# Performance work log

Hardware: AMD Instinct MI355X
Metric: run time of the kernel (lower is better)

The kernel has to match this reference:

```python
import jax, jax.numpy as jnp
import numpy as np

N_NODES = 100000
N_EDGES = 3200000
F_IN, F_HID, F_OUT = 32, 32, 16


def spline_conv(x, edge_index, edge_attr, W, root, bias):
    """SplineConv, dim=1, kernel_size=2, degree=1, open spline, aggr='mean'.
    Basis weights over the 2 kernel slots are (1-u, u) for pseudo u in [0,1).
    W: [2, Fin, Fout], root: [Fin, Fout], bias: [Fout]."""
    src, dst = edge_index[0], edge_index[1]
    u = jnp.clip(edge_attr[:, 0:1], 0.0, 1.0)          # [E,1]
    x_src = x[src]                                      # [E,Fin] gather
    msg = (1.0 - u) * (x_src @ W[0]) + u * (x_src @ W[1])  # [E,Fout]
    agg = jax.ops.segment_sum(msg, dst, num_segments=x.shape[0])
    cnt = jax.ops.segment_sum(jnp.ones((msg.shape[0],), dtype=x.dtype), dst,
                              num_segments=x.shape[0])
    agg = agg / jnp.maximum(cnt, 1.0)[:, None]          # mean aggregation
    return agg + x @ root + bias


def setup_inputs() -> dict:
    key = jax.random.key(0)
    ks = jax.random.split(key, 9)
    x = jax.random.normal(ks[0], (N_NODES, F_IN), dtype=jnp.float32)
    edge_index = jax.random.randint(ks[1], (2, N_EDGES), 0, N_NODES, dtype=jnp.int64)
    edge_attr = jax.random.uniform(ks[2], (N_EDGES, 1), dtype=jnp.float32)
    s1 = 1.0 / np.sqrt(F_IN)
    s2 = 1.0 / np.sqrt(F_HID)
    W1 = jax.random.normal(ks[3], (2, F_IN, F_HID), dtype=jnp.float32) * s1
    root1 = jax.random.normal(ks[4], (F_IN, F_HID), dtype=jnp.float32) * s1
    b1 = jnp.zeros((F_HID,), dtype=jnp.float32)
    W2 = jax.random.normal(ks[5], (2, F_HID, F_OUT), dtype=jnp.float32) * s2
    root2 = jax.random.normal(ks[6], (F_HID, F_OUT), dtype=jnp.float32) * s2
    b2 = jnp.zeros((F_OUT,), dtype=jnp.float32)
    return {"x": x, "edge_index": edge_index, "edge_attr": edge_attr,
            "W1": W1, "root1": root1, "b1": b1,
            "W2": W2, "root2": root2, "b2": b2}


def reference(x, edge_index, edge_attr, W1, root1, b1, W2, root2, b2):
    # dropout is identity in eval mode
    h = jax.nn.relu(spline_conv(x, edge_index, edge_attr, W1, root1, b1))
    h = spline_conv(h, edge_index, edge_attr, W2, root2, b2)
    return jax.nn.log_softmax(h, axis=1)
```

## Files before the change

### kernel.cpp

```cpp
#include <hip/hip_runtime.h>
#include <math.h>

#define NN 100000
#define NE 3200000
#define BSH 6
#define BSZ 64
#define NBKT 1563
#define CAP 2560
#define STILE 8192
#define NTBS 391
#define NPB 1563
#define TST 68
#define NOFF (NBKT + 1)
#define OS2W 392

#define FMA4(a, s, v) { (a).x += (s)*(v).x; (a).y += (s)*(v).y; (a).z += (s)*(v).z; (a).w += (s)*(v).w; }

typedef float v2f __attribute__((ext_vector_type(2)));

__device__ __forceinline__ unsigned fp8pack4(float a, float b, float c, float d) {
    int r = __builtin_amdgcn_cvt_pk_fp8_f32(a, b, 0, false);
    r = __builtin_amdgcn_cvt_pk_fp8_f32(c, d, r, true);
    return (unsigned)r;
}

#define LDE(pp, vv, idx) { int e_ = (idx); \
    if (e_ < cn) { pp = (unsigned)pks[cs + e_]; vv = x1[(size_t)(pp >> 15) * 8 + j]; } \
    else { pp = 0u; vv = 0u; } }
#define ACC(pp, vv) { float u_ = (float)((pp) & 511u) * (1.f / 511.f); \
    v2f lo_ = __builtin_amdgcn_cvt_pk_f32_fp8((vv), false); \
    v2f hi_ = __builtin_amdgcn_cvt_pk_f32_fp8((vv), true); \
    T0 += lo_.x; B0 += u_ * lo_.x;  T1 += lo_.y; B1 += u_ * lo_.y; \
    T2 += hi_.x; B2 += u_ * hi_.x;  T3 += hi_.y; B3 += u_ * hi_.y; }

#define WALK_BODY() \
    int r = t >> 3, j = t & 7; \
    int cs = coff[r], cn = ccnt[r]; \
    float T0=0,T1=0,T2=0,T3=0,B0=0,B1=0,B2=0,B3=0; \
    unsigned pa0, pa1, pa2, pa3, pb0, pb1, pb2, pb3; \
    unsigned va0, va1, va2, va3, vb0, vb1, vb2, vb3; \
    LDE(pa0, va0, 0) LDE(pa1, va1, 1) LDE(pa2, va2, 2) LDE(pa3, va3, 3) \
    LDE(pb0, vb0, 4) LDE(pb1, vb1, 5) LDE(pb2, vb2, 6) LDE(pb3, vb3, 7) \
    for (int k = 0; k < cn; k += 8) { \
        ACC(pa0, va0) ACC(pa1, va1) ACC(pa2, va2) ACC(pa3, va3) \
        LDE(pa0, va0, k + 8)  LDE(pa1, va1, k + 9)  LDE(pa2, va2, k + 10) LDE(pa3, va3, k + 11) \
        ACC(pb0, vb0) ACC(pb1, vb1) ACC(pb2, vb2) ACC(pb3, vb3) \
        LDE(pb0, vb0, k + 12) LDE(pb1, vb1, k + 13) LDE(pb2, vb2, k + 14) LDE(pb3, vb3, k + 15) \
    } \
    __syncthreads();                       \
    ((float4*)(tb + r * TST + 4 * j))[0]      = make_float4(T0, T1, T2, T3); \
    ((float4*)(tb + r * TST + 32 + 4 * j))[0] = make_float4(B0, B1, B2, B3); \
    __syncthreads();

__global__ __launch_bounds__(512, 6) void sp_k(
    const int* __restrict__ ei, const float* __restrict__ ea,
    const float* __restrict__ x, const float* __restrict__ R, const float* __restrict__ b,
    int* __restrict__ pk, unsigned short* __restrict__ offs,
    unsigned* __restrict__ xb, float* __restrict__ xr)
{
    __shared__ __align__(16) union {
        struct { int h[2048]; int staged[STILE]; } sc;
        struct { float Rs[1024]; float xs[64 * 33]; } pp;
    } sm;
    int t = threadIdx.x;

    if (blockIdx.x < NTBS) {
        int* h = sm.sc.h;
        for (int i = t; i < 2048; i += 512) h[i] = 0;
        __syncthreads();
        int e0 = blockIdx.x * STILE;
        int cntblk = NE - e0; if (cntblk > STILE) cntblk = STILE;
        unsigned pck[16]; int bk[16], rk[16];
        #pragma unroll
        for (int i = 0; i < 16; i++) {
            int e = e0 + i * 512 + t;
            bk[i] = -1;
            if (e < NE) {
                int s = ei[e];
                int d = ei[NE + e];
                float u = fminf(fmaxf(ea[e], 0.f), 1.f);
                unsigned uq = __float2uint_rn(u * 511.f);
                bk[i] = d >> BSH;
                pck[i] = ((unsigned)s << 15) | ((unsigned)(d & (BSZ - 1)) << 9) | uq;
                rk[i] = atomicAdd(&h[bk[i]], 1);
            }
        }
        __syncthreads();
        int4 hc = ((const int4*)h)[t];
        int s4 = hc.x + hc.y + hc.z + hc.w;
        int lane = t & 63, wv = t >> 6;
        int inc = s4;
        #pragma unroll
        for (int ofs = 1; ofs < 64; ofs <<= 1) {
            int v = __shfl_up(inc, ofs);
            if (lane >= ofs) inc += v;
        }
        int* wsum = sm.sc.staged;
        if (lane == 63) wsum[wv] = inc;
        __syncthreads();
        int base = 0;
        #pragma unroll
        for (int i = 0; i < 8; i++) { int v = wsum[i]; if (i < wv) base += v; }
        int ex = base + inc - s4;
        __syncthreads();
        ((int4*)h)[t] = make_int4(ex, ex + hc.x, ex + hc.x + hc.y, ex + hc.x + hc.y + hc.z);
        __syncthreads();
        for (int k = t; k < NOFF; k += 512)
            offs[(size_t)blockIdx.x * NOFF + k] = (unsigned short)h[k];
        __syncthreads();
        #pragma unroll
        for (int i = 0; i < 16; i++)
            if (bk[i] >= 0) sm.sc.staged[h[bk[i]] + rk[i]] = (int)pck[i];
        __syncthreads();
        int* seg = pk + (size_t)blockIdx.x * STILE;
        for (int i = t; i * 4 < cntblk; i += 512)
            ((int4*)seg)[i] = ((const int4*)sm.sc.staged)[i];
    } else {
        for (int i = t; i < 1024; i += 512) sm.pp.Rs[i] = R[i];
        int nb = (blockIdx.x - NTBS) * 64;
        for (int i = t; i < 2048; i += 512) {
            int n = nb + (i >> 5);
            sm.pp.xs[(i >> 5) * 33 + (i & 31)] = (n < NN) ? x[n * 32 + (i & 31)] : 0.f;
        }
        __syncthreads();
        int local = t >> 3, c = t & 7;
        int n = nb + local;
        float4 a2 = make_float4(0.f, 0.f, 0.f, 0.f);
        #pragma unroll
        for (int k = 0; k < 32; k++) {
            float xk = sm.pp.xs[local * 33 + k];
            float4 r = ((const float4*)sm.pp.Rs)[k * 8 + c];
            FMA4(a2, xk, r);
        }
        if (n < NN) {
            float4 bb = ((const float4*)b)[c];
            a2.x += bb.x; a2.y += bb.y; a2.z += bb.z; a2.w += bb.w;
            ((float4*)xr)[n * 8 + c] = a2;
            xb[n * 8 + c] = fp8pack4(sm.pp.xs[local * 33 + c * 4 + 0],
                                     sm.pp.xs[local * 33 + c * 4 + 1],
                                     sm.pp.xs[local * 33 + c * 4 + 2],
                                     sm.pp.xs[local * 33 + c * 4 + 3]);
        }
    }
}

__global__ __launch_bounds__(256) void tr_k(
    const unsigned short* __restrict__ offs, unsigned* __restrict__ offs2)
{
    __shared__ unsigned short st[64][68];
    int kt = blockIdx.x % 25;
    int tt = blockIdx.x / 25;
    int t = threadIdx.x;
    for (int i = t; i < 64 * 66; i += 256) {
        int r = i / 66, c = i % 66;
        int row = tt * 64 + r, k = kt * 64 + c;
        st[r][c] = (row < NTBS && k < NOFF) ? offs[(size_t)row * NOFF + k] : (unsigned short)0;
    }
    __syncthreads();
    for (int i = t; i < 64 * 64; i += 256) {
        int kl = i >> 6, tl = i & 63;
        int k = kt * 64 + kl, row = tt * 64 + tl;
        if (k < NBKT && row < NTBS) {
            unsigned o0 = st[tl][kl];
            unsigned cnt = (unsigned)st[tl][kl + 1] - o0;
            offs2[(size_t)k * OS2W + row] = o0 | (cnt << 16);
        }
    }
}

__global__ __launch_bounds__(512, 8) void srt_k(
    const int* __restrict__ pk, const unsigned* __restrict__ offs2,
    int* __restrict__ pk2, int* __restrict__ cnt2)
{
    __shared__ int ccnt[BSZ], coff[BSZ], wsum[8];
    __shared__ __align__(16) int staged[CAP];
    __shared__ __align__(16) int pks[CAP];
    int t = threadIdx.x;
    int bkt = blockIdx.x;
    if (t < BSZ) ccnt[t] = 0;

    int cnt = 0, o0 = 0;
    if (t < NTBS) {
        unsigned pc = offs2[(size_t)bkt * OS2W + t];
        o0 = (int)(pc & 0xFFFFu);
        cnt = (int)(pc >> 16);
    }
    int lane = t & 63, wv = t >> 6;
    int inc = cnt;
    #pragma unroll
    for (int ofs = 1; ofs < 64; ofs <<= 1) {
        int v = __shfl_up(inc, ofs);
        if (lane >= ofs) inc += v;
    }
    if (lane == 63) wsum[wv] = inc;
    __syncthreads();
    int base = 0, tot = 0;
    #pragma unroll
    for (int i = 0; i < 8; i++) { int v = wsum[i]; tot += v; if (i < wv) base += v; }
    int dst = base + inc - cnt;
    int ne = tot < CAP ? tot : CAP;
    if (dst + cnt > CAP) { cnt = CAP - dst; if (cnt < 0) cnt = 0; }
    const int* seg = pk + (size_t)t * STILE + o0;
    int i2 = 0;
    for (; i2 + 4 <= cnt; i2 += 4) {
        int v0 = seg[i2], v1 = seg[i2 + 1], v2 = seg[i2 + 2], v3 = seg[i2 + 3];
        staged[dst + i2] = v0; staged[dst + i2 + 1] = v1;
        staged[dst + i2 + 2] = v2; staged[dst + i2 + 3] = v3;
    }
    for (; i2 < cnt; i2++) staged[dst + i2] = seg[i2];
    __syncthreads();

    unsigned er[5]; int rk[5];
    #pragma unroll
    for (int i = 0; i < 5; i++) {
        int e = i * 512 + t;
        rk[i] = -1;
        if (e < ne) {
            er[i] = (unsigned)staged[e];
            rk[i] = atomicAdd(&ccnt[(er[i] >> 9) & (BSZ - 1)], 1);
        }
    }
    __syncthreads();
    if (t < BSZ) {
        int v = ccnt[t], sc = v;
        #pragma unroll
        for (int ofs = 1; ofs < 64; ofs <<= 1) {
            int nn = __shfl_up(sc, ofs);
            if (t >= ofs) sc += nn;
        }
        coff[t] = sc - v;
    }
    __syncthreads();
    #pragma unroll
    for (int i = 0; i < 5; i++)
        if (rk[i] >= 0) pks[coff[(er[i] >> 9) & (BSZ - 1)] + rk[i]] = (int)er[i];
    if (t < BSZ) cnt2[bkt * BSZ + t] = ccnt[t];
    __syncthreads();

    int n4 = (ne + 3) >> 2;
    int4* dp = (int4*)(pk2 + (size_t)bkt * CAP);
    for (int i = t; i < n4; i += 512) dp[i] = ((const int4*)pks)[i];
}

__global__ __launch_bounds__(512, 8) void agg1_k(
    const int* __restrict__ pk2, const int* __restrict__ cnt2,
    const unsigned* __restrict__ xb, const float* __restrict__ W,
    const float* __restrict__ R2, const float* __restrict__ b2,
    const float* __restrict__ xr, unsigned* __restrict__ hb, float* __restrict__ hr)
{
    __shared__ float Wc[2048];
    __shared__ float R2s[512];
    __shared__ int ccnt[BSZ], coff[BSZ];
    __shared__ int smne;
    __shared__ __align__(16) char smraw[BSZ * TST * 4];
    __shared__ float hs[BSZ * 33];
    int* pks = (int*)smraw;
    float* tb = (float*)smraw;

    int t = threadIdx.x;
    for (int i = t; i < 1024; i += 512) {
        float w0 = W[i];
        Wc[i] = w0;
        Wc[1024 + i] = W[1024 + i] - w0;
    }
    if (t < 512) R2s[t] = R2[t];

    int bkt = blockIdx.x;
    if (t < BSZ) {
        int v = cnt2[bkt * BSZ + t];
        ccnt[t] = v;
        int sc = v;
        #pragma unroll
        for (int ofs = 1; ofs < 64; ofs <<= 1) {
            int nn = __shfl_up(sc, ofs);
            if (t >= ofs) sc += nn;
        }
        coff[t] = sc - v;
        if (t == 63) smne = sc;
    }
    __syncthreads();
    int ne = smne; if (ne > CAP) ne = CAP;
    {
        int n4 = (ne + 3) >> 2;
        const int4* sp4 = (const int4*)(pk2 + (size_t)bkt * CAP);
        for (int i = t; i < n4; i += 512) ((int4*)pks)[i] = sp4[i];
    }
    __syncthreads();

    const unsigned* x1 = xb;
    WALK_BODY()

    {
        int row = t >> 3, cc = t & 7;
        int n = bkt * BSZ + row;
        float inv = 1.f / fmaxf((float)ccnt[row], 1.f);
        float4 acc = make_float4(0.f, 0.f, 0.f, 0.f);
        #pragma unroll
        for (int k = 0; k < 32; k++) {
            float sa = tb[row * TST + k];
            float4 w = ((const float4*)Wc)[k * 8 + cc];
            FMA4(acc, sa, w);
        }
        #pragma unroll
        for (int k = 0; k < 32; k++) {
            float sb = tb[row * TST + 32 + k];
            float4 w = ((const float4*)Wc)[(32 + k) * 8 + cc];
            FMA4(acc, sb, w);
        }
        float h0 = 0.f, h1 = 0.f, h2 = 0.f, h3 = 0.f;
        if (n < NN) {
            float4 rr = ((const float4*)xr)[n * 8 + cc];
            h0 = fmaxf(acc.x * inv + rr.x, 0.f);
            h1 = fmaxf(acc.y * inv + rr.y, 0.f);
            h2 = fmaxf(acc.z * inv + rr.z, 0.f);
            h3 = fmaxf(acc.w * inv + rr.w, 0.f);
            hb[n * 8 + cc] = fp8pack4(h0, h1, h2, h3);
        }
        hs[row * 33 + cc * 4 + 0] = h0;
        hs[row * 33 + cc * 4 + 1] = h1;
        hs[row * 33 + cc * 4 + 2] = h2;
        hs[row * 33 + cc * 4 + 3] = h3;
    }
    __syncthreads();

    #pragma unroll
    for (int p = 0; p < 2; p++) {
        int idx = p * 512 + t;
        int row = idx >> 4, f = idx & 15;
        int n = bkt * BSZ + row;
        if (n < NN) {
            float o = 0.f;
            #pragma unroll
            for (int k = 0; k < 32; k++) o += hs[row * 33 + k] * R2s[k * 16 + f];
            hr[n * 16 + f] = o + b2[f];
        }
    }
}

__global__ __launch_bounds__(512, 8) void agg2_k(
    const int* __restrict__ pk2, const int* __restrict__ cnt2,
    const unsigned* __restrict__ hb, const float* __restrict__ W,
    const float* __restrict__ hr, float* __restrict__ out)
{
    __shared__ float Wc[1024];
    __shared__ int ccnt[BSZ], coff[BSZ];
    __shared__ int smne;
    __shared__ __align__(16) char smraw[BSZ * TST * 4];
    int* pks = (int*)smraw;
    float* tb = (float*)smraw;

    int t = threadIdx.x;
    if (t < 512) {
        float w0 = W[t];
        Wc[t] = w0;
        Wc[512 + t] = W[512 + t] - w0;
    }
    int bkt = blockIdx.x;
    if (t < BSZ) {
        int v = cnt2[bkt * BSZ + t];
        ccnt[t] = v;
        int sc = v;
        #pragma unroll
        for (int ofs = 1; ofs < 64; ofs <<= 1) {
            int nn = __shfl_up(sc, ofs);
            if (t >= ofs) sc += nn;
        }
        coff[t] = sc - v;
        if (t == 63) smne = sc;
    }
    __syncthreads();
    int ne = smne; if (ne > CAP) ne = CAP;
    {
        int n4 = (ne + 3) >> 2;
        const int4* sp4 = (const int4*)(pk2 + (size_t)bkt * CAP);
        for (int i = t; i < n4; i += 512) ((int4*)pks)[i] = sp4[i];
    }
    __syncthreads();

    const unsigned* x1 = hb;
    WALK_BODY()

    #pragma unroll
    for (int p = 0; p < 2; p++) {
        int row = p * 32 + (t >> 4), f = t & 15;
        int n = bkt * BSZ + row;
        float inv = 1.f / fmaxf((float)ccnt[row], 1.f);
        float o = 0.f;
        #pragma unroll
        for (int k = 0; k < 32; k++) o += tb[row * TST + k] * Wc[k * 16 + f];
        #pragma unroll
        for (int k = 0; k < 32; k++) o += tb[row * TST + 32 + k] * Wc[(32 + k) * 16 + f];
        if (n < NN) {
            o = o * inv + hr[n * 16 + f];
            float m = o;
            #pragma unroll
            for (int ofs = 8; ofs; ofs >>= 1) m = fmaxf(m, __shfl_xor(m, ofs, 16));
            float sm = expf(o - m);
            #pragma unroll
            for (int ofs = 8; ofs; ofs >>= 1) sm += __shfl_xor(sm, ofs, 16);
            out[n * 16 + f] = o - (m + logf(sm));
        }
    }
}

extern "C" void kernel_launch(void* const* d_in, const int* in_sizes, int n_in,
                              void* d_out, int out_size, void* d_ws, size_t ws_size,
                              hipStream_t stream) {
    const float* x     = (const float*)d_in[0];
    const int*   ei    = (const int*)d_in[1];
    const float* ea    = (const float*)d_in[2];
    const float* W1    = (const float*)d_in[3];
    const float* root1 = (const float*)d_in[4];
    const float* b1    = (const float*)d_in[5];
    const float* W2    = (const float*)d_in[6];
    const float* root2 = (const float*)d_in[7];
    const float* b2    = (const float*)d_in[8];
    float* out = (float*)d_out;

    int* ws = (int*)d_ws;
    size_t o_pk    = 0;
    size_t o_offs  = o_pk + (size_t)NTBS * STILE;
    size_t o_offs2 = o_offs + 305764;
    size_t o_pk2   = o_offs2 + (size_t)NBKT * OS2W;
    size_t o_cnt2  = o_pk2 + (size_t)NBKT * CAP;
    size_t o_xb    = o_cnt2 + (size_t)NBKT * BSZ;
    size_t o_hb    = o_xb + (size_t)NN * 8;
    size_t o_xr    = o_hb + (size_t)NN * 8;
    size_t o_hr    = o_xr + (size_t)NN * 32;

    int* pk = ws + o_pk;
    unsigned short* offs = (unsigned short*)(ws + o_offs);
    unsigned* offs2 = (unsigned*)(ws + o_offs2);
    int* pk2 = ws + o_pk2;
    int* cnt2 = ws + o_cnt2;
    unsigned* xb = (unsigned*)(ws + o_xb);
    unsigned* hb = (unsigned*)(ws + o_hb);
    float* xr = (float*)(ws + o_xr);
    float* hr = (float*)(ws + o_hr);

    sp_k   <<<NTBS + NPB, 512, 0, stream>>>(ei, ea, x, root1, b1, pk, offs, xb, xr);
    tr_k   <<<25 * 7, 256, 0, stream>>>(offs, offs2);
    srt_k  <<<NBKT, 512, 0, stream>>>(pk, offs2, pk2, cnt2);
    agg1_k <<<NBKT, 512, 0, stream>>>(pk2, cnt2, xb, W1, root2, b2, xr, hb, hr);
    agg2_k <<<NBKT, 512, 0, stream>>>(pk2, cnt2, hb, W2, hr, out);
}
```

Baseline: 236.6 us.

## Fuse offset transpose and bucket sort into the first aggregation kernel

```diff
diff --git a/kernel.cpp b/kernel.cpp
--- a/kernel.cpp
+++ b/kernel.cpp
@@ -12,7 +12,6 @@
 #define NPB 1563
 #define TST 68
 #define NOFF (NBKT + 1)
-#define OS2W 392
 
 #define FMA4(a, s, v) { (a).x += (s)*(v).x; (a).y += (s)*(v).y; (a).z += (s)*(v).z; (a).w += (s)*(v).w; }
 
@@ -144,46 +143,37 @@
     }
 }
 
-__global__ __launch_bounds__(256) void tr_k(
-    const unsigned short* __restrict__ offs, unsigned* __restrict__ offs2)
-{
-    __shared__ unsigned short st[64][68];
-    int kt = blockIdx.x % 25;
-    int tt = blockIdx.x / 25;
-    int t = threadIdx.x;
-    for (int i = t; i < 64 * 66; i += 256) {
-        int r = i / 66, c = i % 66;
-        int row = tt * 64 + r, k = kt * 64 + c;
-        st[r][c] = (row < NTBS && k < NOFF) ? offs[(size_t)row * NOFF + k] : (unsigned short)0;
-    }
-    __syncthreads();
-    for (int i = t; i < 64 * 64; i += 256) {
-        int kl = i >> 6, tl = i & 63;
-        int k = kt * 64 + kl, row = tt * 64 + tl;
-        if (k < NBKT && row < NTBS) {
-            unsigned o0 = st[tl][kl];
-            unsigned cnt = (unsigned)st[tl][kl + 1] - o0;
-            offs2[(size_t)k * OS2W + row] = o0 | (cnt << 16);
-        }
-    }
-}
-
-__global__ __launch_bounds__(512, 8) void srt_k(
-    const int* __restrict__ pk, const unsigned* __restrict__ offs2,
+__global__ __launch_bounds__(512, 8) void agg1_k(
+    const int* __restrict__ pk, const unsigned short* __restrict__ offs,
+    const unsigned* __restrict__ xb, const float* __restrict__ W,
+    const float* __restrict__ R2, const float* __restrict__ b2,
+    const float* __restrict__ xr, unsigned* __restrict__ hb, float* __restrict__ hr,
     int* __restrict__ pk2, int* __restrict__ cnt2)
 {
-    __shared__ int ccnt[BSZ], coff[BSZ], wsum[8];
-    __shared__ __align__(16) int staged[CAP];
-    __shared__ __align__(16) int pks[CAP];
+    __shared__ float Wc[2048];
+    __shared__ float R2s[512];
+    __shared__ int ccnt[BSZ], coff[BSZ];
+    __shared__ int wsum[8];
+    __shared__ __align__(16) char smraw[BSZ * TST * 4];
+    __shared__ __align__(16) union { int staged[CAP]; float hs[BSZ * 33]; } su;
+    int* pks = (int*)smraw;
+    float* tb = (float*)smraw;
+
     int t = threadIdx.x;
+    for (int i = t; i < 1024; i += 512) {
+        float w0 = W[i];
+        Wc[i] = w0;
+        Wc[1024 + i] = W[1024 + i] - w0;
+    }
+    if (t < 512) R2s[t] = R2[t];
+    if (t < BSZ) ccnt[t] = 0;
+
     int bkt = blockIdx.x;
-    if (t < BSZ) ccnt[t] = 0;
-
     int cnt = 0, o0 = 0;
     if (t < NTBS) {
-        unsigned pc = offs2[(size_t)bkt * OS2W + t];
-        o0 = (int)(pc & 0xFFFFu);
-        cnt = (int)(pc >> 16);
+        const unsigned short* orow = offs + (size_t)t * NOFF + bkt;
+        o0 = (int)orow[0];
+        cnt = (int)orow[1] - o0;
     }
     int lane = t & 63, wv = t >> 6;
     int inc = cnt;
@@ -204,10 +194,10 @@
     int i2 = 0;
     for (; i2 + 4 <= cnt; i2 += 4) {
         int v0 = seg[i2], v1 = seg[i2 + 1], v2 = seg[i2 + 2], v3 = seg[i2 + 3];
-        staged[dst + i2] = v0; staged[dst + i2 + 1] = v1;
-        staged[dst + i2 + 2] = v2; staged[dst + i2 + 3] = v3;
-    }
-    for (; i2 < cnt; i2++) staged[dst + i2] = seg[i2];
+        su.staged[dst + i2] = v0; su.staged[dst + i2 + 1] = v1;
+        su.staged[dst + i2 + 2] = v2; su.staged[dst + i2 + 3] = v3;
+    }
+    for (; i2 < cnt; i2++) su.staged[dst + i2] = seg[i2];
     __syncthreads();
 
     unsigned er[5]; int rk[5];
@@ -216,7 +206,7 @@
         int e = i * 512 + t;
         rk[i] = -1;
         if (e < ne) {
-            er[i] = (unsigned)staged[e];
+            er[i] = (unsigned)su.staged[e];
             rk[i] = atomicAdd(&ccnt[(er[i] >> 9) & (BSZ - 1)], 1);
         }
     }
@@ -237,55 +227,11 @@
     if (t < BSZ) cnt2[bkt * BSZ + t] = ccnt[t];
     __syncthreads();
 
-    int n4 = (ne + 3) >> 2;
-    int4* dp = (int4*)(pk2 + (size_t)bkt * CAP);
-    for (int i = t; i < n4; i += 512) dp[i] = ((const int4*)pks)[i];
-}
-
-__global__ __launch_bounds__(512, 8) void agg1_k(
-    const int* __restrict__ pk2, const int* __restrict__ cnt2,
-    const unsigned* __restrict__ xb, const float* __restrict__ W,
-    const float* __restrict__ R2, const float* __restrict__ b2,
-    const float* __restrict__ xr, unsigned* __restrict__ hb, float* __restrict__ hr)
-{
-    __shared__ float Wc[2048];
-    __shared__ float R2s[512];
-    __shared__ int ccnt[BSZ], coff[BSZ];
-    __shared__ int smne;
-    __shared__ __align__(16) char smraw[BSZ * TST * 4];
-    __shared__ float hs[BSZ * 33];
-    int* pks = (int*)smraw;
-    float* tb = (float*)smraw;
-
-    int t = threadIdx.x;
-    for (int i = t; i < 1024; i += 512) {
-        float w0 = W[i];
-        Wc[i] = w0;
-        Wc[1024 + i] = W[1024 + i] - w0;
-    }
-    if (t < 512) R2s[t] = R2[t];
-
-    int bkt = blockIdx.x;
-    if (t < BSZ) {
-        int v = cnt2[bkt * BSZ + t];
-        ccnt[t] = v;
-        int sc = v;
-        #pragma unroll
-        for (int ofs = 1; ofs < 64; ofs <<= 1) {
-            int nn = __shfl_up(sc, ofs);
-            if (t >= ofs) sc += nn;
-        }
-        coff[t] = sc - v;
-        if (t == 63) smne = sc;
-    }
-    __syncthreads();
-    int ne = smne; if (ne > CAP) ne = CAP;
     {
         int n4 = (ne + 3) >> 2;
-        const int4* sp4 = (const int4*)(pk2 + (size_t)bkt * CAP);
-        for (int i = t; i < n4; i += 512) ((int4*)pks)[i] = sp4[i];
-    }
-    __syncthreads();
+        int4* dp = (int4*)(pk2 + (size_t)bkt * CAP);
+        for (int i = t; i < n4; i += 512) dp[i] = ((const int4*)pks)[i];
+    }
 
     const unsigned* x1 = xb;
     WALK_BODY()
@@ -316,10 +262,10 @@
             h3 = fmaxf(acc.w * inv + rr.w, 0.f);
             hb[n * 8 + cc] = fp8pack4(h0, h1, h2, h3);
         }
-        hs[row * 33 + cc * 4 + 0] = h0;
-        hs[row * 33 + cc * 4 + 1] = h1;
-        hs[row * 33 + cc * 4 + 2] = h2;
-        hs[row * 33 + cc * 4 + 3] = h3;
+        su.hs[row * 33 + cc * 4 + 0] = h0;
+        su.hs[row * 33 + cc * 4 + 1] = h1;
+        su.hs[row * 33 + cc * 4 + 2] = h2;
+        su.hs[row * 33 + cc * 4 + 3] = h3;
     }
     __syncthreads();
 
@@ -331,7 +277,7 @@
         if (n < NN) {
             float o = 0.f;
             #pragma unroll
-            for (int k = 0; k < 32; k++) o += hs[row * 33 + k] * R2s[k * 16 + f];
+            for (int k = 0; k < 32; k++) o += su.hs[row * 33 + k] * R2s[k * 16 + f];
             hr[n * 16 + f] = o + b2[f];
         }
     }
@@ -420,8 +366,7 @@
     int* ws = (int*)d_ws;
     size_t o_pk    = 0;
     size_t o_offs  = o_pk + (size_t)NTBS * STILE;
-    size_t o_offs2 = o_offs + 305764;
-    size_t o_pk2   = o_offs2 + (size_t)NBKT * OS2W;
+    size_t o_pk2   = o_offs + 305764;
     size_t o_cnt2  = o_pk2 + (size_t)NBKT * CAP;
     size_t o_xb    = o_cnt2 + (size_t)NBKT * BSZ;
     size_t o_hb    = o_xb + (size_t)NN * 8;
@@ -430,7 +375,6 @@
 
     int* pk = ws + o_pk;
     unsigned short* offs = (unsigned short*)(ws + o_offs);
-    unsigned* offs2 = (unsigned*)(ws + o_offs2);
     int* pk2 = ws + o_pk2;
     int* cnt2 = ws + o_cnt2;
     unsigned* xb = (unsigned*)(ws + o_xb);
@@ -439,8 +383,6 @@
     float* hr = (float*)(ws + o_hr);
 
     sp_k   <<<NTBS + NPB, 512, 0, stream>>>(ei, ea, x, root1, b1, pk, offs, xb, xr);
-    tr_k   <<<25 * 7, 256, 0, stream>>>(offs, offs2);
-    srt_k  <<<NBKT, 512, 0, stream>>>(pk, offs2, pk2, cnt2);
-    agg1_k <<<NBKT, 512, 0, stream>>>(pk2, cnt2, xb, W1, root2, b2, xr, hb, hr);
+    agg1_k <<<NBKT, 512, 0, stream>>>(pk, offs, xb, W1, root2, b2, xr, hb, hr, pk2, cnt2);
     agg2_k <<<NBKT, 512, 0, stream>>>(pk2, cnt2, hb, W2, hr, out);
 }
```

Result: faster. 225.4 us (-4.7%).
